# Kernel optimization log

Measured on AMD Instinct MI355X. Metric: run time of the kernel, lower is better.

The kernel has to match this reference:

```python
import jax, jax.numpy as jnp
import numpy as np

NUM_HEADS = 8
EPS_NORM = 1e-12
EPS_DEN = 1e-5


def _l2norm(x):
    # torch F.normalize(dim=-1): x / max(||x||_2, eps)
    n = jnp.sqrt(jnp.sum(x * x, axis=-1, keepdims=True))
    return x / jnp.maximum(n, EPS_NORM)


def _fast_attention(qs, ks, vs):
    # qs, ks, vs: (B', L, H, m) where L is the attended axis length
    qs = _l2norm(qs)
    ks = _l2norm(ks)
    L = qs.shape[1]
    # KV outer-product summed over the attended axis: (B', H, m, d)
    kvs = jnp.einsum('blhm,blhd->bhmd', ks, vs)
    num = jnp.einsum('bnhm,bhmd->bnhd', qs, kvs) + L * vs
    ks_sum = jnp.sum(ks, axis=1)                       # (B', H, m)
    den = jnp.einsum('bnhm,bhm->bnh', qs, ks_sum)[..., None] + L
    den = jnp.maximum(den, EPS_DEN)                    # clamp_min
    return num / den                                   # (B', L, H, m)


def setup_inputs() -> dict:
    key = jax.random.key(0)
    k1, k2, k3, k4 = jax.random.split(key, 4)
    B, T, N, D = 4, 24, 2048, 256
    x = jax.random.normal(k1, (B, T, N, D), dtype=jnp.float32)
    w_qkv = jax.random.normal(k2, (3 * D, D), dtype=jnp.float32) / np.sqrt(D)
    w_out = jax.random.normal(k3, (D, 2 * D), dtype=jnp.float32) / np.sqrt(2 * D)
    b_out = jax.random.normal(k4, (D,), dtype=jnp.float32) * 0.01
    return {"x": x, "w_qkv": w_qkv, "w_out": w_out, "b_out": b_out}


def reference(x, w_qkv, w_out, b_out):
    B, T, N, D = x.shape
    H = NUM_HEADS
    hd = D // H
    qkv = jnp.einsum('btnd,ed->btne', x, w_qkv)        # (B,T,N,3D), no bias
    q, k, v = jnp.split(qkv, 3, axis=-1)
    # heads: split last dim into (H, hd) chunks == reshape
    qh = q.reshape(B, T, N, H, hd)
    kh = k.reshape(B, T, N, H, hd)
    vh = v.reshape(B, T, N, H, hd)

    # spatial attention: attend over N, batch over (B*T)
    out_s = _fast_attention(qh.reshape(B * T, N, H, hd),
                            kh.reshape(B * T, N, H, hd),
                            vh.reshape(B * T, N, H, hd))
    out_s = out_s.reshape(B, T, N, D)

    # temporal attention: attend over T, batch over (B*N)
    qt = jnp.transpose(qh, (0, 2, 1, 3, 4)).reshape(B * N, T, H, hd)
    kt = jnp.transpose(kh, (0, 2, 1, 3, 4)).reshape(B * N, T, H, hd)
    vt = jnp.transpose(vh, (0, 2, 1, 3, 4)).reshape(B * N, T, H, hd)
    out_t = _fast_attention(qt, kt, vt).reshape(B, N, T, D)
    out_t = jnp.transpose(out_t, (0, 2, 1, 3))         # (B,T,N,D)

    out = jnp.concatenate([out_s, out_t], axis=-1)     # (B,T,N,2D)
    return jnp.einsum('btnf,df->btnd', out, w_out) + b_out
```

## Files before the change

### kernel.cpp

```cpp
#include <hip/hip_runtime.h>
#include <hip/hip_bf16.h>
#include <cstdint>
#include <cstddef>

#define B_   4
#define T_   24
#define NN_  2048
#define D_   256
#define H_   8
#define HD_  32
#define BT_  (B_*T_)
#define MTOK (B_*T_*NN_)

using bf16 = __hip_bfloat16;

typedef __attribute__((ext_vector_type(8))) short bf16x8;
typedef __attribute__((ext_vector_type(4))) float f32x4;

__device__ __forceinline__ float bf2f(bf16 v) { return __bfloat162float(v); }

__device__ __forceinline__ void async_copy16(const void* g, void* l) {
  __builtin_amdgcn_global_load_lds(
      (const __attribute__((address_space(1))) void*)g,
      (__attribute__((address_space(3))) void*)l,
      16, 0, 0);
}

__device__ __forceinline__ float red32(float v) {
  v += __shfl_xor(v, 1, 64);
  v += __shfl_xor(v, 2, 64);
  v += __shfl_xor(v, 4, 64);
  v += __shfl_xor(v, 8, 64);
  v += __shfl_xor(v, 16, 64);
  return v;
}

__global__ void k_convert(const float* __restrict__ in, bf16* __restrict__ out, int n4) {
  int i = blockIdx.x * blockDim.x + threadIdx.x;
  if (i < n4) {
    float4 v = ((const float4*)in)[i];
    bf16 t[4] = {__float2bfloat16(v.x), __float2bfloat16(v.y),
                 __float2bfloat16(v.z), __float2bfloat16(v.w)};
    ((ushort4*)out)[i] = *(ushort4*)t;
  }
}

template<int KD, bool OUTF32>
__global__ __launch_bounds__(256, 2)
void k_gemm(const bf16* __restrict__ A, const bf16* __restrict__ Bw,
            void* __restrict__ Cout, const float* __restrict__ bias, int ncols) {
  __shared__ bf16 As[128 * 64];
  __shared__ bf16 Bs[128 * 64];
  const int tid  = threadIdx.x;
  const int wave = tid >> 6, lane = tid & 63;
  const int quad = lane >> 4, l16 = lane & 15;
  const long row0 = (long)blockIdx.x * 128;
  const long col0 = (long)blockIdx.y * 128;
  const int wm = (wave & 1) * 64, wn = (wave >> 1) * 64;
  const int srow = lane >> 3;
  const int skb  = (lane & 7) * 8;

  f32x4 acc[4][4];
  const f32x4 z = {0.f, 0.f, 0.f, 0.f};
#pragma unroll
  for (int a = 0; a < 4; ++a)
#pragma unroll
    for (int b = 0; b < 4; ++b) acc[a][b] = z;

  for (int k0 = 0; k0 < KD; k0 += 64) {
#pragma unroll
    for (int i = 0; i < 4; ++i) {
      const int c = wave * 4 + i;
      const int r = c * 8 + srow;
      async_copy16(A  + (row0 + r) * KD + k0 + skb, (char*)As + c * 1024);
      async_copy16(Bw + (col0 + r) * KD + k0 + skb, (char*)Bs + c * 1024);
    }
    __syncthreads();
#pragma unroll
    for (int kk = 0; kk < 64; kk += 32) {
      bf16x8 af[4], bfr[4];
#pragma unroll
      for (int i = 0; i < 4; ++i)
        af[i] = *(const bf16x8*)(As + (wm + i * 16 + l16) * 64 + kk + quad * 8);
#pragma unroll
      for (int i = 0; i < 4; ++i)
        bfr[i] = *(const bf16x8*)(Bs + (wn + i * 16 + l16) * 64 + kk + quad * 8);
#pragma unroll
      for (int mi = 0; mi < 4; ++mi)
#pragma unroll
        for (int ni = 0; ni < 4; ++ni)
          acc[mi][ni] = __builtin_amdgcn_mfma_f32_16x16x32_bf16(af[mi], bfr[ni], acc[mi][ni], 0, 0, 0);
    }
    __syncthreads();
  }

#pragma unroll
  for (int mi = 0; mi < 4; ++mi)
#pragma unroll
    for (int ni = 0; ni < 4; ++ni) {
      const long colg = col0 + wn + ni * 16 + l16;
#pragma unroll
      for (int r = 0; r < 4; ++r) {
        const long rowg = row0 + wm + mi * 16 + quad * 4 + r;
        const float v = acc[mi][ni][r];
        if (OUTF32) {
          ((float*)Cout)[rowg * ncols + colg] = v + bias[colg];
        } else {
          ((bf16*)Cout)[rowg * ncols + colg] = __float2bfloat16(v);
        }
      }
    }
}

__global__ __launch_bounds__(256)
void k_spatial_stats(const bf16* __restrict__ qkv, float* __restrict__ stats) {
  const int bt = blockIdx.x, h = blockIdx.y;
  const int tid = threadIdx.x;
  const int wave = tid >> 6, lane = tid & 63;
  __shared__ float lk[256][36];
  __shared__ float lv[256][36];
  const int mg = lane >> 3, dg = lane & 7;
  const int m0 = mg * 4, d0 = dg * 4;
  float acc[4][4] = {};
  float ssum[4] = {0.f, 0.f, 0.f, 0.f};

  for (int c = wave * 64; c < NN_; c += 256) {
    const size_t row = ((size_t)bt * NN_ + c + lane) * 768;
    bf16 kb[32], vb[32];
    const uint4* kp = (const uint4*)(qkv + row + 256 + h * 32);
    const uint4* vp = (const uint4*)(qkv + row + 512 + h * 32);
#pragma unroll
    for (int j = 0; j < 4; ++j) { ((uint4*)kb)[j] = kp[j]; ((uint4*)vb)[j] = vp[j]; }
    float kf[32]; float ss = 0.f;
#pragma unroll
    for (int j = 0; j < 32; ++j) { kf[j] = bf2f(kb[j]); ss += kf[j] * kf[j]; }
    const float sc = 1.f / fmaxf(sqrtf(ss), 1e-12f);
#pragma unroll
    for (int j = 0; j < 32; ++j) kf[j] *= sc;
    float vf[32];
#pragma unroll
    for (int j = 0; j < 32; ++j) vf[j] = bf2f(vb[j]);
    const int lrow = wave * 64 + lane;
#pragma unroll
    for (int j = 0; j < 8; ++j) {
      ((float4*)lk[lrow])[j] = ((float4*)kf)[j];
      ((float4*)lv[lrow])[j] = ((float4*)vf)[j];
    }
    __syncthreads();
#pragma unroll 2
    for (int t = 0; t < 64; ++t) {
      const int tr = wave * 64 + t;
      const float4 ka = *(const float4*)&lk[tr][m0];
      const float4 va = *(const float4*)&lv[tr][d0];
      const float km[4] = {ka.x, ka.y, ka.z, ka.w};
      const float vm[4] = {va.x, va.y, va.z, va.w};
#pragma unroll
      for (int i = 0; i < 4; ++i) {
        ssum[i] += km[i];
#pragma unroll
        for (int j = 0; j < 4; ++j) acc[i][j] += km[i] * vm[j];
      }
    }
    __syncthreads();
  }

  float* rbuf = (float*)lk;
  float* wb = rbuf + wave * 1056;
#pragma unroll
  for (int i = 0; i < 4; ++i) {
    float4 o = {acc[i][0], acc[i][1], acc[i][2], acc[i][3]};
    *(float4*)&wb[(m0 + i) * 32 + d0] = o;
  }
  if (dg == 0) {
#pragma unroll
    for (int i = 0; i < 4; ++i) wb[1024 + m0 + i] = ssum[i];
  }
  __syncthreads();
  float* base = stats + ((size_t)bt * H_ + h) * 1056;
  for (int e = tid; e < 1056; e += 256)
    base[e] = rbuf[e] + rbuf[1056 + e] + rbuf[2112 + e] + rbuf[3168 + e];
}

#define TCH 32
__global__ __launch_bounds__(256, 3)
void k_spatial_out(const bf16* __restrict__ qkv, const float* __restrict__ stats,
                   bf16* __restrict__ concat) {
  const int c  = blockIdx.x;
  const int bt = blockIdx.y;
  const int tid = threadIdx.x;
  const int h = tid >> 5, d = tid & 31;
  __shared__ float qhat[TCH][H_][HD_];

  const float* sbase = stats + ((size_t)bt * H_ + h) * 1056;
  float kvcol[32];
#pragma unroll
  for (int m = 0; m < 32; ++m) kvcol[m] = sbase[m * 32 + d];
  const float kssd = sbase[1024 + d];

  const size_t tok0 = (size_t)bt * NN_ + (size_t)c * TCH;

  for (int i = 0; i < TCH; i += 8) {
    float qf[8];
#pragma unroll
    for (int j = 0; j < 8; ++j)
      qf[j] = bf2f(qkv[(tok0 + i + j) * 768 + h * 32 + d]);
#pragma unroll
    for (int j = 0; j < 8; ++j) {
      const float qss = red32(qf[j] * qf[j]);
      qhat[i + j][h][d] = qf[j] * (1.f / fmaxf(sqrtf(qss), 1e-12f));
    }
  }
  __syncthreads();

  for (int i = 0; i < TCH; i += 8) {
    float vf8[8];
#pragma unroll
    for (int j = 0; j < 8; ++j)
      vf8[j] = bf2f(qkv[(tok0 + i + j) * 768 + 512 + h * 32 + d]);
#pragma unroll
    for (int j = 0; j < 8; ++j) {
      float qr[32];
#pragma unroll
      for (int jj = 0; jj < 8; ++jj)
        ((float4*)qr)[jj] = ((const float4*)&qhat[i + j][h][0])[jj];
      float n0 = 0.f, n1 = 0.f, n2 = 0.f, n3 = 0.f;
#pragma unroll
      for (int m = 0; m < 32; m += 4) {
        n0 = fmaf(qr[m],     kvcol[m],     n0);
        n1 = fmaf(qr[m + 1], kvcol[m + 1], n1);
        n2 = fmaf(qr[m + 2], kvcol[m + 2], n2);
        n3 = fmaf(qr[m + 3], kvcol[m + 3], n3);
      }
      const float num = (n0 + n1) + (n2 + n3) + 2048.f * vf8[j];
      const float qo  = qhat[i + j][h][d];
      const float den = fmaxf(red32(qo * kssd) + 2048.f, 1e-5f);
      concat[(tok0 + i + j) * 512 + h * 32 + d] = __float2bfloat16(num / den);
    }
  }
}

__global__ __launch_bounds__(256, 3)
void k_temporal_out(const bf16* __restrict__ qkv, bf16* __restrict__ concat) {
  const int n = blockIdx.x, b = blockIdx.y;
  const int tid = threadIdx.x;
  const int h = tid >> 5, d = tid & 31;
  __shared__ float khat[T_][H_][HD_];
  __shared__ float qhat[T_][H_][HD_];

  const size_t base = ((size_t)b * T_ * NN_ + n) * 768 + h * 32 + d;
  const size_t tstep = (size_t)NN_ * 768;

  float vf[T_], kfa[T_];
#pragma unroll
  for (int t = 0; t < T_; ++t) {
    kfa[t] = bf2f(qkv[base + t * tstep + 256]);
    vf[t]  = bf2f(qkv[base + t * tstep + 512]);
  }

  float kssd = 0.f;
#pragma unroll
  for (int t = 0; t < T_; ++t) {
    const float ss = red32(kfa[t] * kfa[t]);
    const float kh = kfa[t] * (1.f / fmaxf(sqrtf(ss), 1e-12f));
    kssd += kh;
    khat[t][h][d] = kh;
  }

  float qfa[T_];
#pragma unroll
  for (int t = 0; t < T_; ++t) qfa[t] = bf2f(qkv[base + t * tstep]);
#pragma unroll
  for (int t = 0; t < T_; ++t) {
    const float ss = red32(qfa[t] * qfa[t]);
    qhat[t][h][d] = qfa[t] * (1.f / fmaxf(sqrtf(ss), 1e-12f));
  }
  __syncthreads();

  float kvcol[32];
#pragma unroll
  for (int m = 0; m < 32; ++m) kvcol[m] = 0.f;
#pragma unroll 2
  for (int t = 0; t < T_; ++t) {
    float kr[32];
#pragma unroll
    for (int j = 0; j < 8; ++j)
      ((float4*)kr)[j] = ((const float4*)&khat[t][h][0])[j];
    const float v = vf[t];
#pragma unroll
    for (int m = 0; m < 32; ++m) kvcol[m] = fmaf(kr[m], v, kvcol[m]);
  }

#pragma unroll 2
  for (int t = 0; t < T_; ++t) {
    float qr[32];
#pragma unroll
    for (int j = 0; j < 8; ++j)
      ((float4*)qr)[j] = ((const float4*)&qhat[t][h][0])[j];
    float n0 = 0.f, n1 = 0.f, n2 = 0.f, n3 = 0.f;
#pragma unroll
    for (int m = 0; m < 32; m += 4) {
      n0 = fmaf(qr[m],     kvcol[m],     n0);
      n1 = fmaf(qr[m + 1], kvcol[m + 1], n1);
      n2 = fmaf(qr[m + 2], kvcol[m + 2], n2);
      n3 = fmaf(qr[m + 3], kvcol[m + 3], n3);
    }
    const float num = (n0 + n1) + (n2 + n3) + 24.f * vf[t];
    const float qo  = qhat[t][h][d];
    const float den = fmaxf(red32(qo * kssd) + 24.f, 1e-5f);
    const size_t tok = (size_t)(b * T_ + t) * NN_ + n;
    concat[tok * 512 + 256 + h * 32 + d] = __float2bfloat16(num / den);
  }
}

extern "C" void kernel_launch(void* const* d_in, const int* in_sizes, int n_in,
                              void* d_out, int out_size, void* d_ws, size_t ws_size,
                              hipStream_t stream) {
  (void)in_sizes; (void)n_in; (void)out_size; (void)ws_size;
  const float* x     = (const float*)d_in[0];
  const float* w_qkv = (const float*)d_in[1];
  const float* w_out = (const float*)d_in[2];
  const float* b_out = (const float*)d_in[3];
  float* out = (float*)d_out;
  char* ws = (char*)d_ws;

  bf16* concat = (bf16*)(ws);
  bf16* xb     = (bf16*)(ws);
  bf16* qkv    = (bf16*)(ws + 201326592);
  float* stats = (float*)(ws + 503316480);
  bf16* wqkvb  = (bf16*)(ws + 506560512);
  bf16* woutb  = (bf16*)(ws + 506953728);

  k_convert<<<(MTOK * D_ / 4 + 255) / 256, 256, 0, stream>>>(x, xb, MTOK * D_ / 4);
  k_convert<<<(768 * 256 / 4 + 255) / 256, 256, 0, stream>>>(w_qkv, wqkvb, 768 * 256 / 4);
  k_convert<<<(256 * 512 / 4 + 255) / 256, 256, 0, stream>>>(w_out, woutb, 256 * 512 / 4);

  k_gemm<256, false><<<dim3(MTOK / 128, 768 / 128), 256, 0, stream>>>(xb, wqkvb, qkv, nullptr, 768);

  k_spatial_stats<<<dim3(BT_, H_), 256, 0, stream>>>(qkv, stats);

  k_spatial_out<<<dim3(NN_ / TCH, BT_), 256, 0, stream>>>(qkv, stats, concat);
  k_temporal_out<<<dim3(NN_, B_), 256, 0, stream>>>(qkv, concat);

  k_gemm<512, true><<<dim3(MTOK / 128, 256 / 128), 256, 0, stream>>>(concat, woutb, out, b_out, 256);
}
```

Baseline: 1.115 ms.

## Write normalized q/k back to qkv and reuse them in temporal attention

```diff
diff --git a/kernel.cpp b/kernel.cpp
--- a/kernel.cpp
+++ b/kernel.cpp
@@ -18,6 +18,10 @@
 typedef __attribute__((ext_vector_type(4))) float f32x4;
 
 __device__ __forceinline__ float bf2f(bf16 v) { return __bfloat162float(v); }
+__device__ __forceinline__ ushort f2bfu(float x) {
+  bf16 t = __float2bfloat16(x);
+  return *(ushort*)&t;
+}
 
 __device__ __forceinline__ void async_copy16(const void* g, void* l) {
   __builtin_amdgcn_global_load_lds(
@@ -34,6 +38,16 @@
   v += __shfl_xor(v, 16, 64);
   return v;
 }
+
+#define UNPK8(u, F0,F1,F2,F3,F4,F5,F6,F7)                       \
+  const float F0 = __uint_as_float((u).x << 16);                \
+  const float F1 = __uint_as_float((u).x & 0xffff0000u);        \
+  const float F2 = __uint_as_float((u).y << 16);                \
+  const float F3 = __uint_as_float((u).y & 0xffff0000u);        \
+  const float F4 = __uint_as_float((u).z << 16);                \
+  const float F5 = __uint_as_float((u).z & 0xffff0000u);        \
+  const float F6 = __uint_as_float((u).w << 16);                \
+  const float F7 = __uint_as_float((u).w & 0xffff0000u);
 
 __global__ void k_convert(const float* __restrict__ in, bf16* __restrict__ out, int n4) {
   int i = blockIdx.x * blockDim.x + threadIdx.x;
@@ -113,7 +127,7 @@
 }
 
 __global__ __launch_bounds__(256)
-void k_spatial_stats(const bf16* __restrict__ qkv, float* __restrict__ stats) {
+void k_spatial_stats(bf16* __restrict__ qkv, float* __restrict__ stats) {
   const int bt = blockIdx.x, h = blockIdx.y;
   const int tid = threadIdx.x;
   const int wave = tid >> 6, lane = tid & 63;
@@ -137,6 +151,13 @@
     const float sc = 1.f / fmaxf(sqrtf(ss), 1e-12f);
 #pragma unroll
     for (int j = 0; j < 32; ++j) kf[j] *= sc;
+    ushort kh16[32];
+#pragma unroll
+    for (int j = 0; j < 32; ++j) kh16[j] = f2bfu(kf[j]);
+    uint4* dstk = (uint4*)(qkv + row + 256 + h * 32);
+#pragma unroll
+    for (int j = 0; j < 4; ++j) dstk[j] = ((uint4*)kh16)[j];
+
     float vf[32];
 #pragma unroll
     for (int j = 0; j < 32; ++j) vf[j] = bf2f(vb[j]);
@@ -183,19 +204,21 @@
 
 #define TCH 32
 __global__ __launch_bounds__(256, 3)
-void k_spatial_out(const bf16* __restrict__ qkv, const float* __restrict__ stats,
+void k_spatial_out(bf16* __restrict__ qkv, const float* __restrict__ stats,
                    bf16* __restrict__ concat) {
   const int c  = blockIdx.x;
   const int bt = blockIdx.y;
   const int tid = threadIdx.x;
   const int h = tid >> 5, d = tid & 31;
-  __shared__ float qhat[TCH][H_][HD_];
+  __shared__ uint4 qrow4[TCH * 8 * 4];
 
   const float* sbase = stats + ((size_t)bt * H_ + h) * 1056;
   float kvcol[32];
 #pragma unroll
   for (int m = 0; m < 32; ++m) kvcol[m] = sbase[m * 32 + d];
-  const float kssd = sbase[1024 + d];
+  float kss[32];
+#pragma unroll
+  for (int j = 0; j < 8; ++j) ((float4*)kss)[j] = ((const float4*)(sbase + 1024))[j];
 
   const size_t tok0 = (size_t)bt * NN_ + (size_t)c * TCH;
 
@@ -207,7 +230,10 @@
 #pragma unroll
     for (int j = 0; j < 8; ++j) {
       const float qss = red32(qf[j] * qf[j]);
-      qhat[i + j][h][d] = qf[j] * (1.f / fmaxf(sqrtf(qss), 1e-12f));
+      const float qn = qf[j] * (1.f / fmaxf(sqrtf(qss), 1e-12f));
+      const ushort qb = f2bfu(qn);
+      ((ushort*)qrow4)[((i + j) * 8 + h) * 32 + d] = qb;
+      ((ushort*)qkv)[(tok0 + i + j) * 768 + h * 32 + d] = qb;
     }
   }
   __syncthreads();
@@ -219,94 +245,103 @@
       vf8[j] = bf2f(qkv[(tok0 + i + j) * 768 + 512 + h * 32 + d]);
 #pragma unroll
     for (int j = 0; j < 8; ++j) {
-      float qr[32];
-#pragma unroll
-      for (int jj = 0; jj < 8; ++jj)
-        ((float4*)qr)[jj] = ((const float4*)&qhat[i + j][h][0])[jj];
-      float n0 = 0.f, n1 = 0.f, n2 = 0.f, n3 = 0.f;
-#pragma unroll
-      for (int m = 0; m < 32; m += 4) {
-        n0 = fmaf(qr[m],     kvcol[m],     n0);
-        n1 = fmaf(qr[m + 1], kvcol[m + 1], n1);
-        n2 = fmaf(qr[m + 2], kvcol[m + 2], n2);
-        n3 = fmaf(qr[m + 3], kvcol[m + 3], n3);
+      const uint4* r4 = qrow4 + ((i + j) * 8 + h) * 4;
+      float num = 2048.f * vf8[j];
+      float den = 2048.f;
+#pragma unroll
+      for (int cc = 0; cc < 4; ++cc) {
+        const uint4 u = r4[cc];
+        const int m0 = cc * 8;
+        UNPK8(u, f0, f1, f2, f3, f4, f5, f6, f7)
+        num = fmaf(f0, kvcol[m0+0], num); den = fmaf(f0, kss[m0+0], den);
+        num = fmaf(f1, kvcol[m0+1], num); den = fmaf(f1, kss[m0+1], den);
+        num = fmaf(f2, kvcol[m0+2], num); den = fmaf(f2, kss[m0+2], den);
+        num = fmaf(f3, kvcol[m0+3], num); den = fmaf(f3, kss[m0+3], den);
+        num = fmaf(f4, kvcol[m0+4], num); den = fmaf(f4, kss[m0+4], den);
+        num = fmaf(f5, kvcol[m0+5], num); den = fmaf(f5, kss[m0+5], den);
+        num = fmaf(f6, kvcol[m0+6], num); den = fmaf(f6, kss[m0+6], den);
+        num = fmaf(f7, kvcol[m0+7], num); den = fmaf(f7, kss[m0+7], den);
       }
-      const float num = (n0 + n1) + (n2 + n3) + 2048.f * vf8[j];
-      const float qo  = qhat[i + j][h][d];
-      const float den = fmaxf(red32(qo * kssd) + 2048.f, 1e-5f);
+      den = fmaxf(den, 1e-5f);
       concat[(tok0 + i + j) * 512 + h * 32 + d] = __float2bfloat16(num / den);
     }
   }
 }
 
-__global__ __launch_bounds__(256, 3)
+__global__ __launch_bounds__(256, 4)
 void k_temporal_out(const bf16* __restrict__ qkv, bf16* __restrict__ concat) {
   const int n = blockIdx.x, b = blockIdx.y;
   const int tid = threadIdx.x;
+  const int wave = tid >> 6, lane = tid & 63;
   const int h = tid >> 5, d = tid & 31;
-  __shared__ float khat[T_][H_][HD_];
-  __shared__ float qhat[T_][H_][HD_];
-
-  const size_t base = ((size_t)b * T_ * NN_ + n) * 768 + h * 32 + d;
+  __shared__ uint4 rows4[384 * 4];
+
+  {
+    const int rl = lane >> 2, p = lane & 3;
+#pragma unroll
+    for (int q = 0; q < 6; ++q) {
+      const int i = wave * 6 + q;
+      const int R = i * 16 + rl;
+      const int s = (R >= 192) ? 1 : 0;
+      const int tt = (R - s * 192) >> 3;
+      const int hh = R & 7;
+      const size_t tok = ((size_t)b * T_ + tt) * NN_ + n;
+      const size_t e = tok * 768 + (s ? 0 : 256) + hh * 32 + p * 8;
+      async_copy16(qkv + e, (char*)rows4 + i * 1024);
+    }
+  }
+
+  const size_t basev = ((size_t)b * T_ * NN_ + n) * 768 + 512 + h * 32 + d;
   const size_t tstep = (size_t)NN_ * 768;
-
-  float vf[T_], kfa[T_];
+  float vf[T_];
+#pragma unroll
+  for (int t = 0; t < T_; ++t) vf[t] = bf2f(qkv[basev + t * tstep]);
+
+  __syncthreads();
+
+  float kvcol[32], kss[32];
+#pragma unroll
+  for (int m = 0; m < 32; ++m) { kvcol[m] = 0.f; kss[m] = 0.f; }
 #pragma unroll
   for (int t = 0; t < T_; ++t) {
-    kfa[t] = bf2f(qkv[base + t * tstep + 256]);
-    vf[t]  = bf2f(qkv[base + t * tstep + 512]);
-  }
-
-  float kssd = 0.f;
+    const uint4* r4 = rows4 + (t * 8 + h) * 4;
+    const float v = vf[t];
+#pragma unroll
+    for (int cc = 0; cc < 4; ++cc) {
+      const uint4 u = r4[cc];
+      const int m0 = cc * 8;
+      UNPK8(u, f0, f1, f2, f3, f4, f5, f6, f7)
+      kvcol[m0+0] = fmaf(f0, v, kvcol[m0+0]); kss[m0+0] += f0;
+      kvcol[m0+1] = fmaf(f1, v, kvcol[m0+1]); kss[m0+1] += f1;
+      kvcol[m0+2] = fmaf(f2, v, kvcol[m0+2]); kss[m0+2] += f2;
+      kvcol[m0+3] = fmaf(f3, v, kvcol[m0+3]); kss[m0+3] += f3;
+      kvcol[m0+4] = fmaf(f4, v, kvcol[m0+4]); kss[m0+4] += f4;
+      kvcol[m0+5] = fmaf(f5, v, kvcol[m0+5]); kss[m0+5] += f5;
+      kvcol[m0+6] = fmaf(f6, v, kvcol[m0+6]); kss[m0+6] += f6;
+      kvcol[m0+7] = fmaf(f7, v, kvcol[m0+7]); kss[m0+7] += f7;
+    }
+  }
+
 #pragma unroll
   for (int t = 0; t < T_; ++t) {
-    const float ss = red32(kfa[t] * kfa[t]);
-    const float kh = kfa[t] * (1.f / fmaxf(sqrtf(ss), 1e-12f));
-    kssd += kh;
-    khat[t][h][d] = kh;
-  }
-
-  float qfa[T_];
-#pragma unroll
-  for (int t = 0; t < T_; ++t) qfa[t] = bf2f(qkv[base + t * tstep]);
-#pragma unroll
-  for (int t = 0; t < T_; ++t) {
-    const float ss = red32(qfa[t] * qfa[t]);
-    qhat[t][h][d] = qfa[t] * (1.f / fmaxf(sqrtf(ss), 1e-12f));
-  }
-  __syncthreads();
-
-  float kvcol[32];
-#pragma unroll
-  for (int m = 0; m < 32; ++m) kvcol[m] = 0.f;
-#pragma unroll 2
-  for (int t = 0; t < T_; ++t) {
-    float kr[32];
-#pragma unroll
-    for (int j = 0; j < 8; ++j)
-      ((float4*)kr)[j] = ((const float4*)&khat[t][h][0])[j];
-    const float v = vf[t];
-#pragma unroll
-    for (int m = 0; m < 32; ++m) kvcol[m] = fmaf(kr[m], v, kvcol[m]);
-  }
-
-#pragma unroll 2
-  for (int t = 0; t < T_; ++t) {
-    float qr[32];
-#pragma unroll
-    for (int j = 0; j < 8; ++j)
-      ((float4*)qr)[j] = ((const float4*)&qhat[t][h][0])[j];
-    float n0 = 0.f, n1 = 0.f, n2 = 0.f, n3 = 0.f;
-#pragma unroll
-    for (int m = 0; m < 32; m += 4) {
-      n0 = fmaf(qr[m],     kvcol[m],     n0);
-      n1 = fmaf(qr[m + 1], kvcol[m + 1], n1);
-      n2 = fmaf(qr[m + 2], kvcol[m + 2], n2);
-      n3 = fmaf(qr[m + 3], kvcol[m + 3], n3);
-    }
-    const float num = (n0 + n1) + (n2 + n3) + 24.f * vf[t];
-    const float qo  = qhat[t][h][d];
-    const float den = fmaxf(red32(qo * kssd) + 24.f, 1e-5f);
+    const uint4* r4 = rows4 + ((192 + t * 8 + h)) * 4;
+    float num = 24.f * vf[t];
+    float den = 24.f;
+#pragma unroll
+    for (int cc = 0; cc < 4; ++cc) {
+      const uint4 u = r4[cc];
+      const int m0 = cc * 8;
+      UNPK8(u, f0, f1, f2, f3, f4, f5, f6, f7)
+      num = fmaf(f0, kvcol[m0+0], num); den = fmaf(f0, kss[m0+0], den);
+      num = fmaf(f1, kvcol[m0+1], num); den = fmaf(f1, kss[m0+1], den);
+      num = fmaf(f2, kvcol[m0+2], num); den = fmaf(f2, kss[m0+2], den);
+      num = fmaf(f3, kvcol[m0+3], num); den = fmaf(f3, kss[m0+3], den);
+      num = fmaf(f4, kvcol[m0+4], num); den = fmaf(f4, kss[m0+4], den);
+      num = fmaf(f5, kvcol[m0+5], num); den = fmaf(f5, kss[m0+5], den);
+      num = fmaf(f6, kvcol[m0+6], num); den = fmaf(f6, kss[m0+6], den);
+      num = fmaf(f7, kvcol[m0+7], num); den = fmaf(f7, kss[m0+7], den);
+    }
+    den = fmaxf(den, 1e-5f);
     const size_t tok = (size_t)(b * T_ + t) * NN_ + n;
     concat[tok * 512 + 256 + h * 32 + d] = __float2bfloat16(num / den);
   }
```

Result: slower. 1.151 ms (+3.3%).
